# Performance work log

Hardware: AMD Instinct MI355X
Metric: run time of the kernel (lower is better)

The kernel has to match this reference:

```python
import jax, jax.numpy as jnp
import numpy as np

NUM_HEADS = 16
ROPE_THETA = 10000.0


def setup_inputs() -> dict:
    key = jax.random.key(0)
    k1, k2, k3 = jax.random.split(key, 3)
    B, S, D = 2, 2048, 1024
    std_qkv = float(np.sqrt(2.0 / (D + 3 * D)))
    std_out = float(np.sqrt(2.0 / (D + D)))
    return {
        "x": jax.random.normal(k1, (B, S, D), dtype=jnp.float32),
        "qkv_w": jax.random.normal(k2, (3 * D, D), dtype=jnp.float32) * std_qkv,
        "out_w": jax.random.normal(k3, (D, D), dtype=jnp.float32) * std_out,
        "token_positions": jnp.arange(S, dtype=jnp.int32),
    }


def _apply_rope(x, token_positions, theta=ROPE_THETA):
    # x: [B, H, S, d_k], token_positions: [S]
    d_k = x.shape[-1]
    inv_freqs = 1.0 / (theta ** (jnp.arange(0, d_k, 2, dtype=jnp.float32) / d_k))  # [d_k/2]
    angles = token_positions.astype(jnp.float32)[:, None] * inv_freqs[None, :]     # [S, d_k/2]
    cos, sin = jnp.cos(angles), jnp.sin(angles)
    x_even, x_odd = x[..., 0::2], x[..., 1::2]
    r_even = x_even * cos - x_odd * sin
    r_odd = x_even * sin + x_odd * cos
    # interleave back: [..., d_k/2, 2] -> [..., d_k]
    return jnp.stack([r_even, r_odd], axis=-1).reshape(x.shape)


def reference(x, qkv_w, out_w, token_positions):
    B, S, D = x.shape
    H = NUM_HEADS
    d_k = D // H

    qkv = jnp.einsum("bsd,ed->bse", x, qkv_w)                  # [B, S, 3*D]
    qkv = qkv.reshape(B, S, 3, H, d_k)
    q, k, v = (jnp.transpose(qkv[:, :, i], (0, 2, 1, 3)) for i in range(3))  # each [B, H, S, d_k]

    q = _apply_rope(q, token_positions)
    k = _apply_rope(k, token_positions)

    scale = 1.0 / jnp.sqrt(jnp.asarray(d_k, dtype=x.dtype))
    scores = jnp.einsum("bhqd,bhkd->bhqk", q, k) * scale       # [B, H, S, S]
    causal = jnp.tril(jnp.ones((S, S), dtype=bool))
    scores = jnp.where(causal, scores, jnp.asarray(-jnp.inf, dtype=scores.dtype))
    attn = jax.nn.softmax(scores, axis=-1)
    out = jnp.einsum("bhqk,bhkd->bhqd", attn, v)               # [B, H, S, d_k]
    out = jnp.transpose(out, (0, 2, 1, 3)).reshape(B, S, D)    # [B, S, D]
    return jnp.einsum("bsd,ed->bse", out, out_w)               # [B, S, D]
```

## Files before the change

kernel.cpp:

```cpp
#include <hip/hip_runtime.h>

typedef __bf16 bf16x8 __attribute__((ext_vector_type(8)));
typedef float f32x4 __attribute__((ext_vector_type(4)));
typedef unsigned short u16;
typedef u16 u16x8 __attribute__((ext_vector_type(8)));
typedef u16 u16x4 __attribute__((ext_vector_type(4)));
typedef u16 u16x2 __attribute__((ext_vector_type(2)));

__device__ __forceinline__ u16 f2bf(float f) {
    union { float f; unsigned u; } x; x.f = f;
    unsigned r = x.u + 0x7fffu + ((x.u >> 16) & 1u);
    return (u16)(r >> 16);
}
__device__ __forceinline__ bf16x8 as_bf16x8(u16x8 v) {
    return __builtin_bit_cast(bf16x8, v);
}
__device__ __forceinline__ void glds16(const void* g, void* l) {
    __builtin_amdgcn_global_load_lds(
        (const __attribute__((address_space(1))) void*)g,
        (__attribute__((address_space(3))) void*)l, 16, 0, 0);
}
__device__ __forceinline__ int swz(int r) { return (((r & 7) ^ ((r >> 3) & 7)) << 3); }

__global__ __launch_bounds__(256) void f32bf16(const float* __restrict__ in,
                                               u16* __restrict__ out, int n8) {
    int i = blockIdx.x * 256 + threadIdx.x;
    if (i >= n8) return;
    const float4* p = (const float4*)(in + (size_t)i * 8);
    float4 a = p[0], b = p[1];
    u16x8 o;
    o[0] = f2bf(a.x); o[1] = f2bf(a.y); o[2] = f2bf(a.z); o[3] = f2bf(a.w);
    o[4] = f2bf(b.x); o[5] = f2bf(b.y); o[6] = f2bf(b.z); o[7] = f2bf(b.w);
    *(u16x8*)(out + (size_t)i * 8) = o;
}

__global__ __launch_bounds__(256) void gemm128(const u16* __restrict__ A,
                                               const u16* __restrict__ B,
                                               float* __restrict__ C,
                                               int M, int N, int K) {
    __shared__ u16 As[2][4096];
    __shared__ u16 Bs[2][4096];
    const int tid = threadIdx.x, lane = tid & 63, wave = tid >> 6;
    const int m0 = blockIdx.y << 7, n0 = blockIdx.x << 7;
    const int wr = (wave >> 1) << 6, wc = (wave & 1) << 6;
    const int fr = lane & 15, fo = (lane >> 4) << 3;
    const int srow = tid >> 2, scol = (tid & 3) << 3;
    const u16* Ag = A + (size_t)(m0 + srow) * K + scol;
    const u16* Bg = B + (size_t)(n0 + srow) * K + scol;
    u16* AsW = &As[0][0] + (wave << 9);
    u16* BsW = &Bs[0][0] + (wave << 9);
    f32x4 acc[4][4] = {};
    const int nsteps = K >> 5;
    glds16(Ag, AsW);
    glds16(Ag + (size_t)64 * K, AsW + 2048);
    glds16(Bg, BsW);
    glds16(Bg + (size_t)64 * K, BsW + 2048);
    int cur = 0;
    for (int s = 0; s < nsteps; ++s) {
        __syncthreads();
        if (s + 1 < nsteps) {
            const u16* Ap = Ag + (s + 1) * 32;
            const u16* Bp = Bg + (s + 1) * 32;
            const int nb = (cur ^ 1) << 12;
            glds16(Ap, AsW + nb);
            glds16(Ap + (size_t)64 * K, AsW + nb + 2048);
            glds16(Bp, BsW + nb);
            glds16(Bp + (size_t)64 * K, BsW + nb + 2048);
        }
        const u16* Ab = &As[cur][0];
        const u16* Bb = &Bs[cur][0];
        bf16x8 af[4], bfr[4];
        #pragma unroll
        for (int i = 0; i < 4; ++i)
            af[i] = *(const bf16x8*)(Ab + (wr + i * 16 + fr) * 32 + fo);
        #pragma unroll
        for (int i = 0; i < 4; ++i)
            bfr[i] = *(const bf16x8*)(Bb + (wc + i * 16 + fr) * 32 + fo);
        #pragma unroll
        for (int i = 0; i < 4; ++i)
            #pragma unroll
            for (int j = 0; j < 4; ++j)
                acc[i][j] = __builtin_amdgcn_mfma_f32_16x16x32_bf16(af[i], bfr[j], acc[i][j], 0, 0, 0);
        cur ^= 1;
    }
    const int cr = (lane >> 4) << 2, cc = lane & 15;
    #pragma unroll
    for (int i = 0; i < 4; ++i)
        for (int j = 0; j < 4; ++j)
            for (int r = 0; r < 4; ++r)
                C[(size_t)(m0 + wr + i * 16 + cr + r) * N + (n0 + wc + j * 16 + cc)] = acc[i][j][r];
}

__global__ __launch_bounds__(256) void rope_split(const float* __restrict__ qkv,
                                                  const int* __restrict__ pos,
                                                  u16* __restrict__ Qb,
                                                  u16* __restrict__ Kb,
                                                  u16* __restrict__ Vb) {
    int tid = blockIdx.x * 256 + threadIdx.x;
    int t = tid & 31;
    int h = (tid >> 5) & 15;
    int s = (tid >> 9) & 2047;
    int b = tid >> 20;
    const float* row = qkv + (size_t)((b << 11) + s) * 3072;
    float fp  = (float)pos[s];
    float inv = powf(10000.0f, -(float)(2 * t) * (1.0f / 64.0f));
    float angle = fp * inv;
    float sn, cs;
    sincosf(angle, &sn, &cs);
    int off = h * 64 + 2 * t;
    float2 q2 = *(const float2*)(row + off);
    float2 k2 = *(const float2*)(row + 1024 + off);
    float2 v2 = *(const float2*)(row + 2048 + off);
    size_t oidx = (((size_t)(b * 16 + h) * 2048) + s) * 64 + 2 * t;
    const float qs = 0.18033688011112042f;
    u16x2 qo, ko, vo;
    qo[0] = f2bf((q2.x * cs - q2.y * sn) * qs);
    qo[1] = f2bf((q2.x * sn + q2.y * cs) * qs);
    ko[0] = f2bf(k2.x * cs - k2.y * sn);
    ko[1] = f2bf(k2.x * sn + k2.y * cs);
    vo[0] = f2bf(v2.x);
    vo[1] = f2bf(v2.y);
    *(u16x2*)&Qb[oidx] = qo;
    *(u16x2*)&Kb[oidx] = ko;
    *(u16x2*)&Vb[oidx] = vo;
}

__global__ __launch_bounds__(256) void attn_causal(const u16* __restrict__ Q,
                                                   const u16* __restrict__ K,
                                                   const u16* __restrict__ V,
                                                   u16* __restrict__ O) {
    __shared__ u16 Ks[2][4096];
    __shared__ u16 Vt[2][4096];
    __shared__ u16 Ps[4][1024];
    const int tid = threadIdx.x, lane = tid & 63, wave = tid >> 6;
    const int pr = blockIdx.x, h = blockIdx.y, b = blockIdx.z;
    const int S = 2048, H = 16;
    const size_t base = (size_t)(b * H + h) * S * 64;
    const int fr = lane & 15, fo = (lane >> 4) << 3, cr = (lane >> 4) << 2;
    const int srow = tid >> 3, scol = (tid & 7) << 3;
    u16x8 ones_u;
    #pragma unroll
    for (int i = 0; i < 8; ++i) ones_u[i] = 0x3F80;
    const bf16x8 ones = as_bf16x8(ones_u);

    u16x8 kreg[2], vreg[2];
    #pragma unroll
    for (int phase = 0; phase < 2; ++phase) {
        const int qt = phase ? (31 - pr) : pr;
        const int nkt = qt + 1;
        const int qw = (qt << 6) + (wave << 4);
        bf16x8 aq0, aq1;
        {
            const u16* qrow = Q + base + (size_t)(qw + fr) * 64;
            aq0 = as_bf16x8(*(const u16x8*)(qrow + fo));
            aq1 = as_bf16x8(*(const u16x8*)(qrow + 32 + fo));
        }
        f32x4 oacc[4] = {};
        f32x4 lacc = {};
        #pragma unroll
        for (int p = 0; p < 2; ++p) {
            kreg[p] = *(const u16x8*)(K + base + (size_t)(srow + p * 32) * 64 + scol);
            vreg[p] = *(const u16x8*)(V + base + (size_t)(srow + p * 32) * 64 + scol);
        }
        __syncthreads();
        #pragma unroll
        for (int p = 0; p < 2; ++p) {
            const int row = srow + (p << 5);
            *(u16x8*)&Ks[0][row * 64 + (scol ^ swz(row))] = kreg[p];
            const int pos = ((row & 15) << 2) + (row >> 4);
            #pragma unroll
            for (int j = 0; j < 8; ++j) {
                const int d = scol + j;
                Vt[0][d * 64 + (pos ^ swz(d))] = vreg[p][j];
            }
        }
        if (nkt > 1) {
            #pragma unroll
            for (int p = 0; p < 2; ++p) {
                kreg[p] = *(const u16x8*)(K + base + (size_t)(64 + srow + p * 32) * 64 + scol);
                vreg[p] = *(const u16x8*)(V + base + (size_t)(64 + srow + p * 32) * 64 + scol);
            }
        }
        for (int t = 0; t < nkt; ++t) {
            __syncthreads();
            if (t + 1 < nkt) {
                const int bi = (t + 1) & 1;
                #pragma unroll
                for (int p = 0; p < 2; ++p) {
                    const int row = srow + (p << 5);
                    *(u16x8*)&Ks[bi][row * 64 + (scol ^ swz(row))] = kreg[p];
                    const int pos = ((row & 15) << 2) + (row >> 4);
                    #pragma unroll
                    for (int j = 0; j < 8; ++j) {
                        const int d = scol + j;
                        Vt[bi][d * 64 + (pos ^ swz(d))] = vreg[p][j];
                    }
                }
                if (t + 2 < nkt) {
                    #pragma unroll
                    for (int p = 0; p < 2; ++p) {
                        const u16* kp = K + base + (size_t)(((t + 2) << 6) + srow + p * 32) * 64 + scol;
                        const u16* vp = V + base + (size_t)(((t + 2) << 6) + srow + p * 32) * 64 + scol;
                        kreg[p] = *(const u16x8*)kp;
                        vreg[p] = *(const u16x8*)vp;
                    }
                }
            }
            const u16* Kb = &Ks[t & 1][0];
            const u16* Vb = &Vt[t & 1][0];
            const bool diag = (t == nkt - 1);
            const int nch = diag ? wave + 1 : 4;
            f32x4 sacc[4];
            #pragma unroll
            for (int ch = 0; ch < 4; ++ch) {
                if (ch < nch) {
                    const int r = ch * 16 + fr;
                    const int sw = swz(r);
                    bf16x8 bk0 = *(const bf16x8*)&Kb[r * 64 + (fo ^ sw)];
                    bf16x8 bk1 = *(const bf16x8*)&Kb[r * 64 + ((32 + fo) ^ sw)];
                    f32x4 sc = {};
                    sc = __builtin_amdgcn_mfma_f32_16x16x32_bf16(aq0, bk0, sc, 0, 0, 0);
                    sc = __builtin_amdgcn_mfma_f32_16x16x32_bf16(aq1, bk1, sc, 0, 0, 0);
                    sacc[ch] = sc;
                }
            }
            #pragma unroll
            for (int j = 0; j < 4; ++j) {
                const int prow = cr + j;
                u16x4 pk;
                #pragma unroll
                for (int ch = 0; ch < 4; ++ch) {
                    float e = 0.f;
                    if (ch < nch) {
                        if (!(diag && ch == wave && fr > prow)) e = exp2f(sacc[ch][j]);
                    }
                    pk[ch] = f2bf(e);
                }
                *(u16x4*)&Ps[wave][prow * 64 + ((fr << 2) ^ swz(prow))] = pk;
            }
            #pragma unroll
            for (int kk = 0; kk < 2; ++kk) {
                const int pbase = (kk << 5) + fo;
                bf16x8 pa = *(const bf16x8*)&Ps[wave][fr * 64 + (pbase ^ swz(fr))];
                lacc = __builtin_amdgcn_mfma_f32_16x16x32_bf16(pa, ones, lacc, 0, 0, 0);
                #pragma unroll
                for (int tt = 0; tt < 4; ++tt) {
                    const int d = tt * 16 + fr;
                    bf16x8 bv = *(const bf16x8*)&Vb[d * 64 + (pbase ^ swz(d))];
                    oacc[tt] = __builtin_amdgcn_mfma_f32_16x16x32_bf16(pa, bv, oacc[tt], 0, 0, 0);
                }
            }
        }
        f32x4 inv;
        #pragma unroll
        for (int j = 0; j < 4; ++j) inv[j] = 1.f / lacc[j];
        #pragma unroll
        for (int tt = 0; tt < 4; ++tt)
            for (int j = 0; j < 4; ++j)
                O[(size_t)(b * S + qw + cr + j) * 1024 + h * 64 + tt * 16 + fr] =
                    f2bf(oacc[tt][j] * inv[j]);
    }
}

extern "C" void kernel_launch(void* const* d_in, const int* in_sizes, int n_in,
                              void* d_out, int out_size, void* d_ws, size_t ws_size,
                              hipStream_t stream) {
    const float* x     = (const float*)d_in[0];
    const float* qkv_w = (const float*)d_in[1];
    const float* out_w = (const float*)d_in[2];
    const int*   pos   = (const int*)d_in[3];
    float* out = (float*)d_out;

    char* ws = (char*)d_ws;
    float* qkv  = (float*)ws;
    u16*   Qb   = (u16*)(ws + 50331648);
    u16*   Kb   = (u16*)(ws + 58720256);
    u16*   Vb   = (u16*)(ws + 67108864);
    u16*   x16  = (u16*)(ws + 75497472);
    u16*   att16= (u16*)(ws + 75497472);
    u16*   w16  = (u16*)(ws + 83886080);
    u16*   ow16 = (u16*)(ws + 90177536);

    f32bf16<<<2048, 256, 0, stream>>>(x, x16, 524288);
    f32bf16<<<1536, 256, 0, stream>>>(qkv_w, w16, 393216);
    f32bf16<<<512, 256, 0, stream>>>(out_w, ow16, 131072);
    gemm128<<<dim3(24, 32), 256, 0, stream>>>(x16, w16, qkv, 4096, 3072, 1024);
    rope_split<<<8192, 256, 0, stream>>>(qkv, pos, Qb, Kb, Vb);
    attn_causal<<<dim3(16, 16, 2), 256, 0, stream>>>(Qb, Kb, Vb, att16);
    gemm128<<<dim3(8, 32), 256, 0, stream>>>(att16, ow16, out, 4096, 1024, 1024);
}
```

Measured before the change: 142.7 us.

## Pre-transpose V globally, stage K/V via direct LDS loads, remap blocks per XCD

A new vtrans kernel writes V as bf16 already transposed and permuted, so the attention kernel can fill its K and V tiles with asynchronous global-to-LDS loads. This replaces register staging and the scalar per-element LDS transpose writes. The GEMM and attention grids become 1D with a block-index remap that places neighbouring tiles on the same XCD for better L2 reuse. The cost is one extra kernel launch and an extra pass over the V portion of qkv. The glds-based prefetch also no longer overlaps through registers the way the old double buffering did.

```diff
diff --git a/kernel.cpp b/kernel.cpp
--- a/kernel.cpp
+++ b/kernel.cpp
@@ -37,11 +37,13 @@
 __global__ __launch_bounds__(256) void gemm128(const u16* __restrict__ A,
                                                const u16* __restrict__ B,
                                                float* __restrict__ C,
-                                               int M, int N, int K) {
+                                               int N, int K, int nbx) {
     __shared__ u16 As[2][4096];
     __shared__ u16 Bs[2][4096];
     const int tid = threadIdx.x, lane = tid & 63, wave = tid >> 6;
-    const int m0 = blockIdx.y << 7, n0 = blockIdx.x << 7;
+    const int cpx = gridDim.x >> 3;
+    const int nid = (blockIdx.x & 7) * cpx + (blockIdx.x >> 3);
+    const int m0 = (nid / nbx) << 7, n0 = (nid % nbx) << 7;
     const int wr = (wave >> 1) << 6, wc = (wave & 1) << 6;
     const int fr = lane & 15, fo = (lane >> 4) << 3;
     const int srow = tid >> 2, scol = (tid & 3) << 3;
@@ -94,8 +96,7 @@
 __global__ __launch_bounds__(256) void rope_split(const float* __restrict__ qkv,
                                                   const int* __restrict__ pos,
                                                   u16* __restrict__ Qb,
-                                                  u16* __restrict__ Kb,
-                                                  u16* __restrict__ Vb) {
+                                                  u16* __restrict__ Kb) {
     int tid = blockIdx.x * 256 + threadIdx.x;
     int t = tid & 31;
     int h = (tid >> 5) & 15;
@@ -110,40 +111,83 @@
     int off = h * 64 + 2 * t;
     float2 q2 = *(const float2*)(row + off);
     float2 k2 = *(const float2*)(row + 1024 + off);
-    float2 v2 = *(const float2*)(row + 2048 + off);
     size_t oidx = (((size_t)(b * 16 + h) * 2048) + s) * 64 + 2 * t;
     const float qs = 0.18033688011112042f;
-    u16x2 qo, ko, vo;
+    u16x2 qo, ko;
     qo[0] = f2bf((q2.x * cs - q2.y * sn) * qs);
     qo[1] = f2bf((q2.x * sn + q2.y * cs) * qs);
     ko[0] = f2bf(k2.x * cs - k2.y * sn);
     ko[1] = f2bf(k2.x * sn + k2.y * cs);
-    vo[0] = f2bf(v2.x);
-    vo[1] = f2bf(v2.y);
     *(u16x2*)&Qb[oidx] = qo;
     *(u16x2*)&Kb[oidx] = ko;
-    *(u16x2*)&Vb[oidx] = vo;
+}
+
+__global__ __launch_bounds__(256) void vtrans(const float* __restrict__ qkv,
+                                              u16* __restrict__ Vt) {
+    __shared__ u16 lds[64][72];
+    const int t = threadIdx.x;
+    const int st = blockIdx.x, h = blockIdx.y, b = blockIdx.z;
+    const int s0 = st << 6;
+    {
+        const int r = t >> 2, c0 = (t & 3) << 4;
+        const float* src = qkv + (size_t)((b << 11) + s0 + r) * 3072 + 2048 + h * 64 + c0;
+        const float4* p = (const float4*)src;
+        #pragma unroll
+        for (int q = 0; q < 4; ++q) {
+            float4 v = p[q];
+            lds[r][c0 + q * 4 + 0] = f2bf(v.x);
+            lds[r][c0 + q * 4 + 1] = f2bf(v.y);
+            lds[r][c0 + q * 4 + 2] = f2bf(v.z);
+            lds[r][c0 + q * 4 + 3] = f2bf(v.w);
+        }
+    }
+    __syncthreads();
+    const size_t obase = ((size_t)((b << 4) + h) << 17) + (st << 6);
+    #pragma unroll
+    for (int w = 0; w < 2; ++w) {
+        const int q = t + (w << 8);
+        const int d = q >> 3, c = q & 7;
+        u16x8 o;
+        #pragma unroll
+        for (int i = 0; i < 8; ++i) {
+            const int p = (c << 3) + i;
+            const int k = ((p & 3) << 4) + (p >> 2);
+            o[i] = lds[k][d];
+        }
+        *(u16x8*)(Vt + obase + ((size_t)d << 11) + (c << 3)) = o;
+    }
 }
 
 __global__ __launch_bounds__(256) void attn_causal(const u16* __restrict__ Q,
                                                    const u16* __restrict__ K,
-                                                   const u16* __restrict__ V,
+                                                   const u16* __restrict__ Vt,
                                                    u16* __restrict__ O) {
     __shared__ u16 Ks[2][4096];
-    __shared__ u16 Vt[2][4096];
+    __shared__ u16 Vs[2][4096];
     __shared__ u16 Ps[4][1024];
     const int tid = threadIdx.x, lane = tid & 63, wave = tid >> 6;
-    const int pr = blockIdx.x, h = blockIdx.y, b = blockIdx.z;
-    const int S = 2048, H = 16;
-    const size_t base = (size_t)(b * H + h) * S * 64;
+    const int nid = ((blockIdx.x & 7) << 6) + (blockIdx.x >> 3);
+    const int pr = nid & 15, h = (nid >> 4) & 15, b = nid >> 8;
+    const int S = 2048;
+    const size_t base = (size_t)((b << 4) + h) << 17;
     const int fr = lane & 15, fo = (lane >> 4) << 3, cr = (lane >> 4) << 2;
-    const int srow = tid >> 3, scol = (tid & 7) << 3;
+    const int schk = lane & 7, srow8 = lane >> 3;
     u16x8 ones_u;
     #pragma unroll
     for (int i = 0; i < 8; ++i) ones_u[i] = 0x3F80;
     const bf16x8 ones = as_bf16x8(ones_u);
 
-    u16x8 kreg[2], vreg[2];
+    auto stage = [&](int t, int bi) {
+        #pragma unroll
+        for (int g = 0; g < 2; ++g) {
+            const int rg = (wave << 4) + (g << 3);
+            const int r  = rg + srow8;
+            const int ck = (schk ^ srow8 ^ ((wave << 1) + g)) << 3;
+            glds16(K  + base + ((size_t)((t << 6) + r) << 6) + ck, &Ks[bi][rg << 6]);
+            glds16(Vt + base + ((size_t)r << 11) + (t << 6) + ck,   &Vs[bi][rg << 6]);
+        }
+    };
+
     #pragma unroll
     for (int phase = 0; phase < 2; ++phase) {
         const int qt = phase ? (31 - pr) : pr;
@@ -157,57 +201,13 @@
         }
         f32x4 oacc[4] = {};
         f32x4 lacc = {};
-        #pragma unroll
-        for (int p = 0; p < 2; ++p) {
-            kreg[p] = *(const u16x8*)(K + base + (size_t)(srow + p * 32) * 64 + scol);
-            vreg[p] = *(const u16x8*)(V + base + (size_t)(srow + p * 32) * 64 + scol);
-        }
         __syncthreads();
-        #pragma unroll
-        for (int p = 0; p < 2; ++p) {
-            const int row = srow + (p << 5);
-            *(u16x8*)&Ks[0][row * 64 + (scol ^ swz(row))] = kreg[p];
-            const int pos = ((row & 15) << 2) + (row >> 4);
-            #pragma unroll
-            for (int j = 0; j < 8; ++j) {
-                const int d = scol + j;
-                Vt[0][d * 64 + (pos ^ swz(d))] = vreg[p][j];
-            }
-        }
-        if (nkt > 1) {
-            #pragma unroll
-            for (int p = 0; p < 2; ++p) {
-                kreg[p] = *(const u16x8*)(K + base + (size_t)(64 + srow + p * 32) * 64 + scol);
-                vreg[p] = *(const u16x8*)(V + base + (size_t)(64 + srow + p * 32) * 64 + scol);
-            }
-        }
+        stage(0, 0);
         for (int t = 0; t < nkt; ++t) {
             __syncthreads();
-            if (t + 1 < nkt) {
-                const int bi = (t + 1) & 1;
-                #pragma unroll
-                for (int p = 0; p < 2; ++p) {
-                    const int row = srow + (p << 5);
-                    *(u16x8*)&Ks[bi][row * 64 + (scol ^ swz(row))] = kreg[p];
-                    const int pos = ((row & 15) << 2) + (row >> 4);
-                    #pragma unroll
-                    for (int j = 0; j < 8; ++j) {
-                        const int d = scol + j;
-                        Vt[bi][d * 64 + (pos ^ swz(d))] = vreg[p][j];
-                    }
-                }
-                if (t + 2 < nkt) {
-                    #pragma unroll
-                    for (int p = 0; p < 2; ++p) {
-                        const u16* kp = K + base + (size_t)(((t + 2) << 6) + srow + p * 32) * 64 + scol;
-                        const u16* vp = V + base + (size_t)(((t + 2) << 6) + srow + p * 32) * 64 + scol;
-                        kreg[p] = *(const u16x8*)kp;
-                        vreg[p] = *(const u16x8*)vp;
-                    }
-                }
-            }
+            if (t + 1 < nkt) stage(t + 1, (t + 1) & 1);
             const u16* Kb = &Ks[t & 1][0];
-            const u16* Vb = &Vt[t & 1][0];
+            const u16* Vb = &Vs[t & 1][0];
             const bool diag = (t == nkt - 1);
             const int nch = diag ? wave + 1 : 4;
             f32x4 sacc[4];
@@ -275,7 +275,7 @@
     float* qkv  = (float*)ws;
     u16*   Qb   = (u16*)(ws + 50331648);
     u16*   Kb   = (u16*)(ws + 58720256);
-    u16*   Vb   = (u16*)(ws + 67108864);
+    u16*   Vtg  = (u16*)(ws + 67108864);
     u16*   x16  = (u16*)(ws + 75497472);
     u16*   att16= (u16*)(ws + 75497472);
     u16*   w16  = (u16*)(ws + 83886080);
@@ -284,8 +284,9 @@
     f32bf16<<<2048, 256, 0, stream>>>(x, x16, 524288);
     f32bf16<<<1536, 256, 0, stream>>>(qkv_w, w16, 393216);
     f32bf16<<<512, 256, 0, stream>>>(out_w, ow16, 131072);
-    gemm128<<<dim3(24, 32), 256, 0, stream>>>(x16, w16, qkv, 4096, 3072, 1024);
-    rope_split<<<8192, 256, 0, stream>>>(qkv, pos, Qb, Kb, Vb);
-    attn_causal<<<dim3(16, 16, 2), 256, 0, stream>>>(Qb, Kb, Vb, att16);
-    gemm128<<<dim3(8, 32), 256, 0, stream>>>(att16, ow16, out, 4096, 1024, 1024);
-}
+    gemm128<<<768, 256, 0, stream>>>(x16, w16, qkv, 3072, 1024, 24);
+    rope_split<<<8192, 256, 0, stream>>>(qkv, pos, Qb, Kb);
+    vtrans<<<dim3(32, 16, 2), 256, 0, stream>>>(qkv, Vtg);
+    attn_causal<<<512, 256, 0, stream>>>(Qb, Kb, Vtg, att16);
+    gemm128<<<256, 256, 0, stream>>>(att16, ow16, out, 1024, 1024, 8);
+}
```

After: 144.7 us. Within noise of the previous version (+1.3%).
